# Kernel optimization log

Measured on AMD Instinct MI355X. Metric: run time of the kernel, lower is better.

Reference implementation:

```python
import jax, jax.numpy as jnp
import numpy as np

LMAX = 4
NUM_COEF = (LMAX + 1) ** 2  # 25 spherical-harmonic coefficients
EPS = 1e-5
# degree l of each coefficient index m
DEG = np.repeat(np.arange(LMAX + 1), 2 * np.arange(LMAX + 1) + 1)
# degree-balanced weights for layer_norm_sh (std_balance_degrees=True): 1/((2l+1)*lmax)
_BW = np.zeros(NUM_COEF - 1, dtype=np.float32)
for l in range(1, LMAX + 1):
    _BW[l**2 - 1 : l**2 - 1 + 2 * l + 1] = 1.0 / (2 * l + 1)
_BW /= LMAX


def setup_inputs() -> dict:
    N, C, H, O, S = 20000, 64, 64, 64, 64
    key = jax.random.key(0)
    ks = jax.random.split(key, 9)
    def g(k, shape, scale=0.05):
        return jax.random.normal(k, shape, dtype=jnp.float32) * scale
    return {
        'x': jax.random.normal(ks[0], (N, NUM_COEF, C), dtype=jnp.float32),
        'norm_l0_w': jnp.ones((C,), jnp.float32),
        'norm_l0_b': jnp.zeros((C,), jnp.float32),
        'norm_aff_w': jnp.ones((LMAX, C), jnp.float32),
        'lin1_w': g(ks[1], (LMAX + 1, C, H)),
        'lin1_b': jnp.zeros((H,), jnp.float32),
        'scalar_w': g(ks[2], (C, H)),
        'scalar_b': jnp.zeros((H,), jnp.float32),
        'grid_w1': g(ks[3], (H, 2 * H)),
        'grid_w2': g(ks[4], (2 * H, 2 * H)),
        'grid_w3': g(ks[5], (2 * H, H)),
        'lin2_w': g(ks[6], (LMAX + 1, H, O)),
        'lin2_b': jnp.zeros((O,), jnp.float32),
        'to_grid_mat': g(ks[7], (S, NUM_COEF), scale=0.2),
    }


def reference(x, norm_l0_w, norm_l0_b, norm_aff_w, lin1_w, lin1_b,
              scalar_w, scalar_b, grid_w1, grid_w2, grid_w3,
              lin2_w, lin2_b, to_grid_mat):
    deg = jnp.asarray(DEG)
    bw = jnp.asarray(_BW)
    # --- layer_norm_sh (EquivariantLayerNormArraySphericalHarmonics) ---
    x0 = x[:, :1, :]                                   # [N,1,C] l=0 part
    mu = x0.mean(-1, keepdims=True)
    var = ((x0 - mu) ** 2).mean(-1, keepdims=True)
    x0n = (x0 - mu) * jax.lax.rsqrt(var + EPS) * norm_l0_w + norm_l0_b
    xl = x[:, 1:, :]                                   # [N,24,C] l>=1 part
    fnorm = jnp.einsum('nic,i->nc', xl * xl, bw)[:, None, :]   # degree-balanced RMS
    inv = jax.lax.rsqrt(fnorm.mean(-1, keepdims=True) + EPS)   # [N,1,1]
    xl = xl * inv * norm_aff_w[deg[1:] - 1][None]              # per-degree affine
    xn = jnp.concatenate([x0n, xl], axis=1)            # [N,25,C]
    # --- scalar gating MLP on l=0 (use_grid_mlp + use_sep_s2_act) ---
    gating = jax.nn.silu(jnp.einsum('noc,ch->noh', xn[:, :1, :], scalar_w) + scalar_b)
    # --- SO3_LinearV2 #1: per-degree block-diagonal linear ---
    h = jnp.einsum('nmi,mio->nmo', xn, lin1_w[deg])    # [N,25,H]
    h = h.at[:, 0, :].add(lin1_b)
    # --- grid MLP: to S2 grid, pointwise MLP, back to coefficients ---
    g = jnp.einsum('sm,nmh->nsh', to_grid_mat, h)      # [N,S,H]
    g = jax.nn.silu(g @ grid_w1)
    g = jax.nn.silu(g @ grid_w2)
    g = g @ grid_w3
    h = jnp.einsum('sm,nsh->nmh', to_grid_mat, g)      # from_grid_mat == to_grid_mat
    # --- separable S2 activation: replace l=0 row with gated scalars ---
    h = jnp.concatenate([gating, h[:, 1:, :]], axis=1)
    # --- SO3_LinearV2 #2 ---
    out = jnp.einsum('nmi,mio->nmo', h, lin2_w[deg])   # [N,25,O]
    out = out.at[:, 0, :].add(lin2_b)
    return out
```

## Files before the change

kernel.cpp:

```cpp
#include <hip/hip_runtime.h>
#include <hip/hip_bf16.h>

#define EPSV 1e-5f

typedef __attribute__((ext_vector_type(8))) short short8;
typedef __attribute__((ext_vector_type(4))) float f32x4;

__device__ __forceinline__ int deg_of(int m) {
  return (m == 0) ? 0 : (m < 4 ? 1 : (m < 9 ? 2 : (m < 16 ? 3 : 4)));
}
__device__ __forceinline__ float silu_f(float v) { return v / (1.f + __expf(-v)); }
__device__ __forceinline__ unsigned short f2bf(float v) {
  unsigned int u = __float_as_uint(v);
  return (unsigned short)((u + 0x7FFFu + ((u >> 16) & 1u)) >> 16);
}
__device__ __forceinline__ short bfs(float v) { return (short)f2bf(v); }

#define OFF_L1 0
#define OFF_L2 20480
#define OFF_SC 40960
#define OFF_G1 45056
#define OFF_G2 53248
#define OFF_G3 69632
#define OFF_TG 77824
#define OFF_TGT 79872
#define WS_SHORTS 81920

__global__ __launch_bounds__(256) void prep_weights_kernel(
    const float* __restrict__ l1w, const float* __restrict__ l2w,
    const float* __restrict__ scw, const float* __restrict__ gw1,
    const float* __restrict__ gw2, const float* __restrict__ gw3,
    const float* __restrict__ tgm, short* __restrict__ wsh)
{
  int i = blockIdx.x * 256 + threadIdx.x;
  if (i < 20480) {
    int l = i >> 12, r = i & 4095, h = r >> 6, c = r & 63;
    wsh[i] = bfs(l1w[l * 4096 + c * 64 + h]);
  } else if (i < 40960) {
    int r0 = i - OFF_L2;
    int l = r0 >> 12, r = r0 & 4095, o = r >> 6, h = r & 63;
    wsh[i] = bfs(l2w[l * 4096 + h * 64 + o]);
  } else if (i < 45056) {
    int r = i - OFF_SC, h = r >> 6, c = r & 63;
    wsh[i] = bfs(scw[c * 64 + h]);
  } else if (i < 53248) {
    int r = i - OFF_G1, o = r >> 6, h = r & 63;
    wsh[i] = bfs(gw1[h * 128 + o]);
  } else if (i < 69632) {
    int r = i - OFF_G2, o = r >> 7, h = r & 127;
    wsh[i] = bfs(gw2[h * 128 + o]);
  } else if (i < 77824) {
    int r = i - OFF_G3, o = r >> 7, h = r & 127;
    wsh[i] = bfs(gw3[h * 64 + o]);
  } else if (i < 79872) {
    int r = i - OFF_TG, s = r >> 5, m = r & 31;
    wsh[i] = (m < 25) ? bfs(tgm[s * 25 + m]) : (short)0;
  } else if (i < WS_SHORTS) {
    int r = i - OFF_TGT, m = r >> 6, s = r & 63;
    wsh[i] = (m < 25) ? bfs(tgm[s * 25 + m]) : (short)0;
  }
}


__global__ __launch_bounds__(256, 4) void fused_sample_kernel(
    const float* __restrict__ x,
    const float* __restrict__ nl0w, const float* __restrict__ nl0b,
    const float* __restrict__ affw,
    const float* __restrict__ l1b,
    const float* __restrict__ scb,
    const float* __restrict__ l2b,
    const short* __restrict__ wsh,
    float* __restrict__ out, int nTot)
{
  __shared__ float sm[9856];
  float*          XB  = sm;
  unsigned short* T1u = (unsigned short*)sm;
  unsigned short* G3u = (unsigned short*)sm;
  unsigned short* XBh = (unsigned short*)(sm + 4352);
  unsigned short* H1u = (unsigned short*)(sm + 5504);
  unsigned short* GBu = (unsigned short*)(sm + 6784);
  unsigned short* T2u = (unsigned short*)(sm + 4352);
  float*          RD  = sm + 8704;
  unsigned short* HBh = (unsigned short*)(sm + 8704);

  const int t = threadIdx.x;
  const int n = blockIdx.x;
  if (n >= nTot) return;

  const int W    = t >> 6;
  const int lane = t & 63;
  const int quad = lane >> 4;
  const int l16  = lane & 15;
  const int hcol = W * 16 + l16;

  const float* gx = x + (size_t)n * 1600;
  const short8 z8 = (short8){0,0,0,0,0,0,0,0};

  const short* l1T = wsh + OFF_L1;
  const short* l2T = wsh + OFF_L2;
  const short* scT = wsh + OFF_SC;
  const short* g1T = wsh + OFF_G1;
  const short* g2T = wsh + OFF_G2;
  const short* g3T = wsh + OFF_G3;
  const short* tgP = wsh + OFF_TG;
  const short* tgT = wsh + OFF_TGT;

  for (int f = 4 * t; f < 1600; f += 1024) {
    float4 v = *(const float4*)(gx + f);
    int m = f >> 6, c = f & 63;
    *(float4*)(XB + m * 68 + c) = v;
  }
  for (int i = t; i < 448; i += 256) {
    int r = i / 7, k = 25 + i % 7;
    H1u[r * 40 + k] = 0;
  }
  __syncthreads();

  {
    float part = 0.f;
    for (int f = 64 + t; f < 1600; f += 256) {
      int m = f >> 6, c = f & 63;
      float v = XB[m * 68 + c];
      int l = deg_of(m);
      part += v * v * (1.f / (float)((2 * l + 1) * 4));
    }
    RD[t] = part;
  }
  __syncthreads();
  if (t < 64) {
    float s4 = RD[t] + RD[t + 64] + RD[t + 128] + RD[t + 192];
    #pragma unroll
    for (int o = 32; o >= 1; o >>= 1) s4 += __shfl_xor(s4, o, 64);
    if (t == 0) RD[0] = rsqrtf(s4 * (1.f / 64.f) + EPSV);
  } else if (t < 128) {
    int c = t - 64;
    float v = XB[c];
    float s1 = v, s2 = v * v;
    #pragma unroll
    for (int o = 32; o >= 1; o >>= 1) {
      s1 += __shfl_xor(s1, o, 64);
      s2 += __shfl_xor(s2, o, 64);
    }
    float mu  = s1 * (1.f / 64.f);
    float var = s2 * (1.f / 64.f) - mu * mu;
    XB[c] = (v - mu) * rsqrtf(var + EPSV) * nl0w[c] + nl0b[c];
  }
  __syncthreads();

  short8 B3[12];
  {
    #pragma unroll
    for (int l = 0; l < 5; ++l)
      #pragma unroll
      for (int ks = 0; ks < 2; ++ks)
        B3[l * 2 + ks] = *(const short8*)(l1T + l * 4096 + hcol * 64 + ks * 32 + quad * 8);
    #pragma unroll
    for (int ks = 0; ks < 2; ++ks)
      B3[10 + ks] = *(const short8*)(scT + hcol * 64 + ks * 32 + quad * 8);

    float inv = RD[0];
    for (int f = t; f < 1600; f += 256) {
      int m = f >> 6, c = f & 63;
      float v = XB[m * 68 + c];
      if (m > 0) v *= inv * affw[(deg_of(m) - 1) * 64 + c];
      XBh[m * 72 + c] = f2bf(v);
    }
  }
  __syncthreads();

  float gval;
  short8 tg3b;
  {
    tg3b = *(const short8*)(tgP + (W * 16 + l16) * 32 + quad * 8);

    short8 a0[2], a1[2];
    #pragma unroll
    for (int ks = 0; ks < 2; ++ks) {
      a0[ks] = *(const short8*)(XBh + l16 * 72 + ks * 32 + quad * 8);
      a1[ks] = *(const short8*)(XBh + (16 + l16) * 72 + ks * 32 + quad * 8);
    }
    const int dl = deg_of(l16);
    f32x4 c0 = (f32x4){0,0,0,0}, c1 = (f32x4){0,0,0,0}, cg = (f32x4){0,0,0,0};
    #pragma unroll
    for (int ks = 0; ks < 2; ++ks) {
      #pragma unroll
      for (int l = 0; l < 4; ++l) {
        short8 am = (dl == l) ? a0[ks] : z8;
        c0 = __builtin_amdgcn_mfma_f32_16x16x32_bf16(am, B3[l * 2 + ks], c0, 0, 0, 0);
      }
      c1 = __builtin_amdgcn_mfma_f32_16x16x32_bf16(a1[ks], B3[8 + ks], c1, 0, 0, 0);
      short8 ag = (l16 == 0) ? a0[ks] : z8;
      cg = __builtin_amdgcn_mfma_f32_16x16x32_bf16(ag, B3[10 + ks], cg, 0, 0, 0);
    }
    #pragma unroll
    for (int r = 0; r < 4; ++r) {
      int m = quad * 4 + r;
      float v = c0[r] + ((m == 0) ? l1b[hcol] : 0.f);
      H1u[hcol * 40 + m] = f2bf(v);
    }
    #pragma unroll
    for (int r = 0; r < 4; ++r) {
      int m = 16 + quad * 4 + r;
      if (m < 25) H1u[hcol * 40 + m] = f2bf(c1[r]);
    }
    gval = silu_f(cg[0] + scb[hcol]);
  }
  __syncthreads();

  short8 bf4[4];
  {
    #pragma unroll
    for (int nt2 = 0; nt2 < 2; ++nt2)
      #pragma unroll
      for (int ks = 0; ks < 2; ++ks)
        bf4[nt2 * 2 + ks] = *(const short8*)(g1T + ((2 * W + nt2) * 16 + l16) * 64 + ks * 32 + quad * 8);

    f32x4 cg3[4];
    #pragma unroll
    for (int nt = 0; nt < 4; ++nt) cg3[nt] = (f32x4){0,0,0,0};
    #pragma unroll
    for (int nt = 0; nt < 4; ++nt) {
      short8 b = *(const short8*)(H1u + (nt * 16 + l16) * 40 + quad * 8);
      cg3[nt] = __builtin_amdgcn_mfma_f32_16x16x32_bf16(tg3b, b, cg3[nt], 0, 0, 0);
    }
    #pragma unroll
    for (int nt = 0; nt < 4; ++nt)
      #pragma unroll
      for (int r = 0; r < 4; ++r) {
        int s = W * 16 + quad * 4 + r;
        GBu[s * 72 + nt * 16 + l16] = f2bf(cg3[nt][r]);
      }
  }
  __syncthreads();

  short8 bf5[8];
  {
    #pragma unroll
    for (int nt2 = 0; nt2 < 2; ++nt2)
      #pragma unroll
      for (int ks = 0; ks < 4; ++ks)
        bf5[nt2 * 4 + ks] = *(const short8*)(g2T + ((2 * W + nt2) * 16 + l16) * 128 + ks * 32 + quad * 8);

    f32x4 acc[8];
    #pragma unroll
    for (int i = 0; i < 8; ++i) acc[i] = (f32x4){0,0,0,0};
    #pragma unroll
    for (int mt = 0; mt < 4; ++mt)
      #pragma unroll
      for (int ks = 0; ks < 2; ++ks) {
        short8 a = *(const short8*)(GBu + (mt * 16 + l16) * 72 + ks * 32 + quad * 8);
        acc[mt * 2 + 0] = __builtin_amdgcn_mfma_f32_16x16x32_bf16(a, bf4[ks],     acc[mt * 2 + 0], 0, 0, 0);
        acc[mt * 2 + 1] = __builtin_amdgcn_mfma_f32_16x16x32_bf16(a, bf4[2 + ks], acc[mt * 2 + 1], 0, 0, 0);
      }
    #pragma unroll
    for (int mt = 0; mt < 4; ++mt)
      #pragma unroll
      for (int nt2 = 0; nt2 < 2; ++nt2) {
        int col = (2 * W + nt2) * 16 + l16;
        #pragma unroll
        for (int r = 0; r < 4; ++r) {
          int srow = mt * 16 + quad * 4 + r;
          T1u[srow * 136 + col] = f2bf(silu_f(acc[mt * 2 + nt2][r]));
        }
      }
  }
  __syncthreads();

  short8 bf6[4];
  {
    #pragma unroll
    for (int ks = 0; ks < 4; ++ks)
      bf6[ks] = *(const short8*)(g3T + hcol * 128 + ks * 32 + quad * 8);

    f32x4 acc[8];
    #pragma unroll
    for (int i = 0; i < 8; ++i) acc[i] = (f32x4){0,0,0,0};
    #pragma unroll
    for (int mt = 0; mt < 4; ++mt)
      #pragma unroll
      for (int ks = 0; ks < 4; ++ks) {
        short8 a = *(const short8*)(T1u + (mt * 16 + l16) * 136 + ks * 32 + quad * 8);
        acc[mt * 2 + 0] = __builtin_amdgcn_mfma_f32_16x16x32_bf16(a, bf5[ks],     acc[mt * 2 + 0], 0, 0, 0);
        acc[mt * 2 + 1] = __builtin_amdgcn_mfma_f32_16x16x32_bf16(a, bf5[4 + ks], acc[mt * 2 + 1], 0, 0, 0);
      }
    #pragma unroll
    for (int mt = 0; mt < 4; ++mt)
      #pragma unroll
      for (int nt2 = 0; nt2 < 2; ++nt2) {
        int col = (2 * W + nt2) * 16 + l16;
        #pragma unroll
        for (int r = 0; r < 4; ++r) {
          int srow = mt * 16 + quad * 4 + r;
          T2u[srow * 136 + col] = f2bf(silu_f(acc[mt * 2 + nt2][r]));
        }
      }
  }
  __syncthreads();

  short8 a7[2][2];
  {
    #pragma unroll
    for (int mt = 0; mt < 2; ++mt)
      #pragma unroll
      for (int ks = 0; ks < 2; ++ks)
        a7[mt][ks] = *(const short8*)(tgT + (mt * 16 + l16) * 64 + ks * 32 + quad * 8);

    f32x4 acc[4];
    #pragma unroll
    for (int i = 0; i < 4; ++i) acc[i] = (f32x4){0,0,0,0};
    #pragma unroll
    for (int mt = 0; mt < 4; ++mt)
      #pragma unroll
      for (int ks = 0; ks < 4; ++ks) {
        short8 a = *(const short8*)(T2u + (mt * 16 + l16) * 136 + ks * 32 + quad * 8);
        acc[mt] = __builtin_amdgcn_mfma_f32_16x16x32_bf16(a, bf6[ks], acc[mt], 0, 0, 0);
      }
    #pragma unroll
    for (int mt = 0; mt < 4; ++mt)
      #pragma unroll
      for (int r = 0; r < 4; ++r) {
        int s = mt * 16 + quad * 4 + r;
        G3u[hcol * 72 + s] = f2bf(acc[mt][r]);
      }
  }
  __syncthreads();

  short8 B8[10];
  {
    #pragma unroll
    for (int l = 0; l < 5; ++l)
      #pragma unroll
      for (int ks = 0; ks < 2; ++ks)
        B8[l * 2 + ks] = *(const short8*)(l2T + l * 4096 + hcol * 64 + ks * 32 + quad * 8);

    short8 b7[2];
    #pragma unroll
    for (int ks = 0; ks < 2; ++ks)
      b7[ks] = *(const short8*)(G3u + hcol * 72 + ks * 32 + quad * 8);
    f32x4 c7[2];
    #pragma unroll
    for (int mt = 0; mt < 2; ++mt) c7[mt] = (f32x4){0,0,0,0};
    #pragma unroll
    for (int mt = 0; mt < 2; ++mt)
      #pragma unroll
      for (int ks = 0; ks < 2; ++ks)
        c7[mt] = __builtin_amdgcn_mfma_f32_16x16x32_bf16(a7[mt][ks], b7[ks], c7[mt], 0, 0, 0);
    #pragma unroll
    for (int mt = 0; mt < 2; ++mt)
      #pragma unroll
      for (int r = 0; r < 4; ++r) {
        int m = mt * 16 + quad * 4 + r;
        if (m >= 1 && m < 25) HBh[m * 72 + hcol] = f2bf(c7[mt][r]);
      }
    if (quad == 0) HBh[hcol] = f2bf(gval);
  }
  __syncthreads();

  {
    short8 a0[2], a1[2];
    #pragma unroll
    for (int ks = 0; ks < 2; ++ks) {
      a0[ks] = *(const short8*)(HBh + l16 * 72 + ks * 32 + quad * 8);
      a1[ks] = *(const short8*)(HBh + (16 + l16) * 72 + ks * 32 + quad * 8);
    }
    const int dl = deg_of(l16);
    f32x4 c0 = (f32x4){0,0,0,0}, c1 = (f32x4){0,0,0,0};
    #pragma unroll
    for (int ks = 0; ks < 2; ++ks) {
      #pragma unroll
      for (int l = 0; l < 4; ++l) {
        short8 am = (dl == l) ? a0[ks] : z8;
        c0 = __builtin_amdgcn_mfma_f32_16x16x32_bf16(am, B8[l * 2 + ks], c0, 0, 0, 0);
      }
      c1 = __builtin_amdgcn_mfma_f32_16x16x32_bf16(a1[ks], B8[8 + ks], c1, 0, 0, 0);
    }
    float* go = out + (size_t)n * 1600;
    float bias = l2b[hcol];
    #pragma unroll
    for (int r = 0; r < 4; ++r) {
      int m = quad * 4 + r;
      go[m * 64 + hcol] = c0[r] + ((m == 0) ? bias : 0.f);
    }
    #pragma unroll
    for (int r = 0; r < 4; ++r) {
      int m = 16 + quad * 4 + r;
      if (m < 25) go[m * 64 + hcol] = c1[r];
    }
  }
}

extern "C" void kernel_launch(void* const* d_in, const int* in_sizes, int n_in,
                              void* d_out, int out_size, void* d_ws, size_t ws_size,
                              hipStream_t stream) {
  const float* x    = (const float*)d_in[0];
  const float* nl0w = (const float*)d_in[1];
  const float* nl0b = (const float*)d_in[2];
  const float* affw = (const float*)d_in[3];
  const float* l1w  = (const float*)d_in[4];
  const float* l1b  = (const float*)d_in[5];
  const float* scw  = (const float*)d_in[6];
  const float* scb  = (const float*)d_in[7];
  const float* gw1  = (const float*)d_in[8];
  const float* gw2  = (const float*)d_in[9];
  const float* gw3  = (const float*)d_in[10];
  const float* l2w  = (const float*)d_in[11];
  const float* l2b  = (const float*)d_in[12];
  const float* tgm  = (const float*)d_in[13];

  short* wsh = (short*)d_ws;
  int N = in_sizes[0] / 1600;

  prep_weights_kernel<<<dim3(WS_SHORTS / 256), dim3(256), 0, stream>>>(
      l1w, l2w, scw, gw1, gw2, gw3, tgm, wsh);

  fused_sample_kernel<<<dim3(N), dim3(256), 0, stream>>>(
      x, nl0w, nl0b, affw, l1b, scb, l2b, wsh, (float*)d_out, N);
}
```

Measured before the change: 617.2 us.

## Swap MFMA operand roles so outputs pack into vectorized LDS and global stores

Several MFMA stages swap their A and B operands so each lane's four accumulator values land in consecutive columns. Results can then be packed into paired bf16 words and written with 8-byte LDS stores and 16-byte global stores instead of scalar 2-byte and 4-byte stores. The normalization loops are also vectorized to float4 LDS reads. Padding rows of XBh and HBh are zeroed, because the swapped final stage now reads rows 25 to 31 as B operands. This aims to cut LDS store instruction count and improve global write coalescing, at the cost of more careful padding and indexing.

```diff
diff --git a/kernel.cpp b/kernel.cpp
--- a/kernel.cpp
+++ b/kernel.cpp
@@ -5,6 +5,7 @@
 
 typedef __attribute__((ext_vector_type(8))) short short8;
 typedef __attribute__((ext_vector_type(4))) float f32x4;
+typedef __attribute__((ext_vector_type(2))) unsigned int u32x2;
 
 __device__ __forceinline__ int deg_of(int m) {
   return (m == 0) ? 0 : (m < 4 ? 1 : (m < 9 ? 2 : (m < 16 ? 3 : 4)));
@@ -15,6 +16,9 @@
   return (unsigned short)((u + 0x7FFFu + ((u >> 16) & 1u)) >> 16);
 }
 __device__ __forceinline__ short bfs(float v) { return (short)f2bf(v); }
+__device__ __forceinline__ unsigned int pk2(float a, float b) {
+  return (unsigned int)f2bf(a) | ((unsigned int)f2bf(b) << 16);
+}
 
 #define OFF_L1 0
 #define OFF_L2 20480
@@ -114,15 +118,25 @@
     int r = i / 7, k = 25 + i % 7;
     H1u[r * 40 + k] = 0;
   }
+  for (int i = t; i < 504; i += 256)
+    XBh[25 * 72 + i] = 0;
+  for (int i = t; i < 504; i += 256)
+    HBh[25 * 72 + i] = 0;
   __syncthreads();
 
   {
     float part = 0.f;
-    for (int f = 64 + t; f < 1600; f += 256) {
-      int m = f >> 6, c = f & 63;
-      float v = XB[m * 68 + c];
-      int l = deg_of(m);
-      part += v * v * (1.f / (float)((2 * l + 1) * 4));
+    #pragma unroll
+    for (int it = 0; it < 2; ++it) {
+      int i = t + it * 256;
+      if (i < 384) {
+        int f = 64 + 4 * i;
+        int m = f >> 6, c = f & 63;
+        f32x4 v = *(const f32x4*)(XB + m * 68 + c);
+        int l = deg_of(m);
+        float w = 1.f / (float)((2 * l + 1) * 4);
+        part += (v[0]*v[0] + v[1]*v[1] + v[2]*v[2] + v[3]*v[3]) * w;
+      }
     }
     RD[t] = part;
   }
@@ -159,11 +173,20 @@
       B3[10 + ks] = *(const short8*)(scT + hcol * 64 + ks * 32 + quad * 8);
 
     float inv = RD[0];
-    for (int f = t; f < 1600; f += 256) {
-      int m = f >> 6, c = f & 63;
-      float v = XB[m * 68 + c];
-      if (m > 0) v *= inv * affw[(deg_of(m) - 1) * 64 + c];
-      XBh[m * 72 + c] = f2bf(v);
+    #pragma unroll
+    for (int it = 0; it < 2; ++it) {
+      int i = t + it * 256;
+      if (i < 400) {
+        int m = i >> 4, c = (i & 15) * 4;
+        f32x4 v = *(const f32x4*)(XB + m * 68 + c);
+        if (m > 0) {
+          f32x4 aw = *(const f32x4*)(affw + (deg_of(m) - 1) * 64 + c);
+          v[0] *= inv * aw[0]; v[1] *= inv * aw[1];
+          v[2] *= inv * aw[2]; v[3] *= inv * aw[3];
+        }
+        u32x2 w; w[0] = pk2(v[0], v[1]); w[1] = pk2(v[2], v[3]);
+        *(u32x2*)(XBh + m * 72 + c) = w;
+      }
     }
   }
   __syncthreads();
@@ -192,76 +215,71 @@
       short8 ag = (l16 == 0) ? a0[ks] : z8;
       cg = __builtin_amdgcn_mfma_f32_16x16x32_bf16(ag, B3[10 + ks], cg, 0, 0, 0);
     }
-    #pragma unroll
-    for (int r = 0; r < 4; ++r) {
-      int m = quad * 4 + r;
-      float v = c0[r] + ((m == 0) ? l1b[hcol] : 0.f);
-      H1u[hcol * 40 + m] = f2bf(v);
-    }
-    #pragma unroll
-    for (int r = 0; r < 4; ++r) {
-      int m = 16 + quad * 4 + r;
-      if (m < 25) H1u[hcol * 40 + m] = f2bf(c1[r]);
+    if (quad == 0) c0[0] += l1b[hcol];
+    u32x2 w0; w0[0] = pk2(c0[0], c0[1]); w0[1] = pk2(c0[2], c0[3]);
+    *(u32x2*)(H1u + hcol * 40 + quad * 4) = w0;
+    if (quad < 2) {
+      u32x2 w1; w1[0] = pk2(c1[0], c1[1]); w1[1] = pk2(c1[2], c1[3]);
+      *(u32x2*)(H1u + hcol * 40 + 16 + quad * 4) = w1;
+    } else if (quad == 2) {
+      H1u[hcol * 40 + 24] = f2bf(c1[0]);
     }
     gval = silu_f(cg[0] + scb[hcol]);
   }
   __syncthreads();
 
-  short8 bf4[4];
+  short8 a4w[2][2];
   {
     #pragma unroll
     for (int nt2 = 0; nt2 < 2; ++nt2)
       #pragma unroll
       for (int ks = 0; ks < 2; ++ks)
-        bf4[nt2 * 2 + ks] = *(const short8*)(g1T + ((2 * W + nt2) * 16 + l16) * 64 + ks * 32 + quad * 8);
+        a4w[nt2][ks] = *(const short8*)(g1T + ((2 * W + nt2) * 16 + l16) * 64 + ks * 32 + quad * 8);
 
     f32x4 cg3[4];
     #pragma unroll
     for (int nt = 0; nt < 4; ++nt) cg3[nt] = (f32x4){0,0,0,0};
     #pragma unroll
     for (int nt = 0; nt < 4; ++nt) {
-      short8 b = *(const short8*)(H1u + (nt * 16 + l16) * 40 + quad * 8);
-      cg3[nt] = __builtin_amdgcn_mfma_f32_16x16x32_bf16(tg3b, b, cg3[nt], 0, 0, 0);
-    }
-    #pragma unroll
-    for (int nt = 0; nt < 4; ++nt)
-      #pragma unroll
-      for (int r = 0; r < 4; ++r) {
-        int s = W * 16 + quad * 4 + r;
-        GBu[s * 72 + nt * 16 + l16] = f2bf(cg3[nt][r]);
-      }
-  }
-  __syncthreads();
-
-  short8 bf5[8];
+      short8 ah = *(const short8*)(H1u + (nt * 16 + l16) * 40 + quad * 8);
+      cg3[nt] = __builtin_amdgcn_mfma_f32_16x16x32_bf16(ah, tg3b, cg3[nt], 0, 0, 0);
+    }
+    #pragma unroll
+    for (int nt = 0; nt < 4; ++nt) {
+      u32x2 w; w[0] = pk2(cg3[nt][0], cg3[nt][1]); w[1] = pk2(cg3[nt][2], cg3[nt][3]);
+      *(u32x2*)(GBu + (W * 16 + l16) * 72 + nt * 16 + quad * 4) = w;
+    }
+  }
+  __syncthreads();
+
+  short8 a5w[2][4];
   {
     #pragma unroll
     for (int nt2 = 0; nt2 < 2; ++nt2)
       #pragma unroll
       for (int ks = 0; ks < 4; ++ks)
-        bf5[nt2 * 4 + ks] = *(const short8*)(g2T + ((2 * W + nt2) * 16 + l16) * 128 + ks * 32 + quad * 8);
+        a5w[nt2][ks] = *(const short8*)(g2T + ((2 * W + nt2) * 16 + l16) * 128 + ks * 32 + quad * 8);
 
     f32x4 acc[8];
     #pragma unroll
     for (int i = 0; i < 8; ++i) acc[i] = (f32x4){0,0,0,0};
     #pragma unroll
-    for (int mt = 0; mt < 4; ++mt)
+    for (int st = 0; st < 4; ++st)
       #pragma unroll
       for (int ks = 0; ks < 2; ++ks) {
-        short8 a = *(const short8*)(GBu + (mt * 16 + l16) * 72 + ks * 32 + quad * 8);
-        acc[mt * 2 + 0] = __builtin_amdgcn_mfma_f32_16x16x32_bf16(a, bf4[ks],     acc[mt * 2 + 0], 0, 0, 0);
-        acc[mt * 2 + 1] = __builtin_amdgcn_mfma_f32_16x16x32_bf16(a, bf4[2 + ks], acc[mt * 2 + 1], 0, 0, 0);
-      }
-    #pragma unroll
-    for (int mt = 0; mt < 4; ++mt)
-      #pragma unroll
-      for (int nt2 = 0; nt2 < 2; ++nt2) {
-        int col = (2 * W + nt2) * 16 + l16;
+        short8 b = *(const short8*)(GBu + (st * 16 + l16) * 72 + ks * 32 + quad * 8);
+        acc[0 * 4 + st] = __builtin_amdgcn_mfma_f32_16x16x32_bf16(a4w[0][ks], b, acc[0 * 4 + st], 0, 0, 0);
+        acc[1 * 4 + st] = __builtin_amdgcn_mfma_f32_16x16x32_bf16(a4w[1][ks], b, acc[1 * 4 + st], 0, 0, 0);
+      }
+    #pragma unroll
+    for (int nt2 = 0; nt2 < 2; ++nt2)
+      #pragma unroll
+      for (int st = 0; st < 4; ++st) {
+        f32x4 v = acc[nt2 * 4 + st];
         #pragma unroll
-        for (int r = 0; r < 4; ++r) {
-          int srow = mt * 16 + quad * 4 + r;
-          T1u[srow * 136 + col] = f2bf(silu_f(acc[mt * 2 + nt2][r]));
-        }
+        for (int r = 0; r < 4; ++r) v[r] = silu_f(v[r]);
+        u32x2 w; w[0] = pk2(v[0], v[1]); w[1] = pk2(v[2], v[3]);
+        *(u32x2*)(T1u + (st * 16 + l16) * 136 + (2 * W + nt2) * 16 + quad * 4) = w;
       }
   }
   __syncthreads();
@@ -276,34 +294,33 @@
     #pragma unroll
     for (int i = 0; i < 8; ++i) acc[i] = (f32x4){0,0,0,0};
     #pragma unroll
-    for (int mt = 0; mt < 4; ++mt)
+    for (int st = 0; st < 4; ++st)
       #pragma unroll
       for (int ks = 0; ks < 4; ++ks) {
-        short8 a = *(const short8*)(T1u + (mt * 16 + l16) * 136 + ks * 32 + quad * 8);
-        acc[mt * 2 + 0] = __builtin_amdgcn_mfma_f32_16x16x32_bf16(a, bf5[ks],     acc[mt * 2 + 0], 0, 0, 0);
-        acc[mt * 2 + 1] = __builtin_amdgcn_mfma_f32_16x16x32_bf16(a, bf5[4 + ks], acc[mt * 2 + 1], 0, 0, 0);
-      }
-    #pragma unroll
-    for (int mt = 0; mt < 4; ++mt)
-      #pragma unroll
-      for (int nt2 = 0; nt2 < 2; ++nt2) {
-        int col = (2 * W + nt2) * 16 + l16;
+        short8 b = *(const short8*)(T1u + (st * 16 + l16) * 136 + ks * 32 + quad * 8);
+        acc[0 * 4 + st] = __builtin_amdgcn_mfma_f32_16x16x32_bf16(a5w[0][ks], b, acc[0 * 4 + st], 0, 0, 0);
+        acc[1 * 4 + st] = __builtin_amdgcn_mfma_f32_16x16x32_bf16(a5w[1][ks], b, acc[1 * 4 + st], 0, 0, 0);
+      }
+    #pragma unroll
+    for (int nt2 = 0; nt2 < 2; ++nt2)
+      #pragma unroll
+      for (int st = 0; st < 4; ++st) {
+        f32x4 v = acc[nt2 * 4 + st];
         #pragma unroll
-        for (int r = 0; r < 4; ++r) {
-          int srow = mt * 16 + quad * 4 + r;
-          T2u[srow * 136 + col] = f2bf(silu_f(acc[mt * 2 + nt2][r]));
-        }
-      }
-  }
-  __syncthreads();
-
-  short8 a7[2][2];
+        for (int r = 0; r < 4; ++r) v[r] = silu_f(v[r]);
+        u32x2 w; w[0] = pk2(v[0], v[1]); w[1] = pk2(v[2], v[3]);
+        *(u32x2*)(T2u + (st * 16 + l16) * 136 + (2 * W + nt2) * 16 + quad * 4) = w;
+      }
+  }
+  __syncthreads();
+
+  short8 b7w[2][2];
   {
     #pragma unroll
     for (int mt = 0; mt < 2; ++mt)
       #pragma unroll
       for (int ks = 0; ks < 2; ++ks)
-        a7[mt][ks] = *(const short8*)(tgT + (mt * 16 + l16) * 64 + ks * 32 + quad * 8);
+        b7w[mt][ks] = *(const short8*)(tgT + (mt * 16 + l16) * 64 + ks * 32 + quad * 8);
 
     f32x4 acc[4];
     #pragma unroll
@@ -316,12 +333,10 @@
         acc[mt] = __builtin_amdgcn_mfma_f32_16x16x32_bf16(a, bf6[ks], acc[mt], 0, 0, 0);
       }
     #pragma unroll
-    for (int mt = 0; mt < 4; ++mt)
-      #pragma unroll
-      for (int r = 0; r < 4; ++r) {
-        int s = mt * 16 + quad * 4 + r;
-        G3u[hcol * 72 + s] = f2bf(acc[mt][r]);
-      }
+    for (int mt = 0; mt < 4; ++mt) {
+      u32x2 w; w[0] = pk2(acc[mt][0], acc[mt][1]); w[1] = pk2(acc[mt][2], acc[mt][3]);
+      *(u32x2*)(G3u + hcol * 72 + mt * 16 + quad * 4) = w;
+    }
   }
   __syncthreads();
 
@@ -333,35 +348,32 @@
       for (int ks = 0; ks < 2; ++ks)
         B8[l * 2 + ks] = *(const short8*)(l2T + l * 4096 + hcol * 64 + ks * 32 + quad * 8);
 
-    short8 b7[2];
-    #pragma unroll
-    for (int ks = 0; ks < 2; ++ks)
-      b7[ks] = *(const short8*)(G3u + hcol * 72 + ks * 32 + quad * 8);
     f32x4 c7[2];
-    #pragma unroll
-    for (int mt = 0; mt < 2; ++mt) c7[mt] = (f32x4){0,0,0,0};
-    #pragma unroll
-    for (int mt = 0; mt < 2; ++mt)
-      #pragma unroll
-      for (int ks = 0; ks < 2; ++ks)
-        c7[mt] = __builtin_amdgcn_mfma_f32_16x16x32_bf16(a7[mt][ks], b7[ks], c7[mt], 0, 0, 0);
-    #pragma unroll
-    for (int mt = 0; mt < 2; ++mt)
-      #pragma unroll
-      for (int r = 0; r < 4; ++r) {
-        int m = mt * 16 + quad * 4 + r;
-        if (m >= 1 && m < 25) HBh[m * 72 + hcol] = f2bf(c7[mt][r]);
-      }
+    c7[0] = (f32x4){0,0,0,0}; c7[1] = (f32x4){0,0,0,0};
+    #pragma unroll
+    for (int ks = 0; ks < 2; ++ks) {
+      short8 ag = *(const short8*)(G3u + hcol * 72 + ks * 32 + quad * 8);
+      c7[0] = __builtin_amdgcn_mfma_f32_16x16x32_bf16(ag, b7w[0][ks], c7[0], 0, 0, 0);
+      c7[1] = __builtin_amdgcn_mfma_f32_16x16x32_bf16(ag, b7w[1][ks], c7[1], 0, 0, 0);
+    }
+    if (l16 >= 1) {
+      u32x2 w; w[0] = pk2(c7[0][0], c7[0][1]); w[1] = pk2(c7[0][2], c7[0][3]);
+      *(u32x2*)(HBh + l16 * 72 + W * 16 + quad * 4) = w;
+    }
+    if (l16 < 9) {
+      u32x2 w; w[0] = pk2(c7[1][0], c7[1][1]); w[1] = pk2(c7[1][2], c7[1][3]);
+      *(u32x2*)(HBh + (16 + l16) * 72 + W * 16 + quad * 4) = w;
+    }
     if (quad == 0) HBh[hcol] = f2bf(gval);
   }
   __syncthreads();
 
   {
-    short8 a0[2], a1[2];
+    short8 b0[2], b1[2];
     #pragma unroll
     for (int ks = 0; ks < 2; ++ks) {
-      a0[ks] = *(const short8*)(HBh + l16 * 72 + ks * 32 + quad * 8);
-      a1[ks] = *(const short8*)(HBh + (16 + l16) * 72 + ks * 32 + quad * 8);
+      b0[ks] = *(const short8*)(HBh + l16 * 72 + ks * 32 + quad * 8);
+      b1[ks] = *(const short8*)(HBh + (16 + l16) * 72 + ks * 32 + quad * 8);
     }
     const int dl = deg_of(l16);
     f32x4 c0 = (f32x4){0,0,0,0}, c1 = (f32x4){0,0,0,0};
@@ -369,23 +381,19 @@
     for (int ks = 0; ks < 2; ++ks) {
       #pragma unroll
       for (int l = 0; l < 4; ++l) {
-        short8 am = (dl == l) ? a0[ks] : z8;
-        c0 = __builtin_amdgcn_mfma_f32_16x16x32_bf16(am, B8[l * 2 + ks], c0, 0, 0, 0);
-      }
-      c1 = __builtin_amdgcn_mfma_f32_16x16x32_bf16(a1[ks], B8[8 + ks], c1, 0, 0, 0);
+        short8 bm = (dl == l) ? b0[ks] : z8;
+        c0 = __builtin_amdgcn_mfma_f32_16x16x32_bf16(B8[l * 2 + ks], bm, c0, 0, 0, 0);
+      }
+      c1 = __builtin_amdgcn_mfma_f32_16x16x32_bf16(B8[8 + ks], b1[ks], c1, 0, 0, 0);
     }
     float* go = out + (size_t)n * 1600;
-    float bias = l2b[hcol];
-    #pragma unroll
-    for (int r = 0; r < 4; ++r) {
-      int m = quad * 4 + r;
-      go[m * 64 + hcol] = c0[r] + ((m == 0) ? bias : 0.f);
-    }
-    #pragma unroll
-    for (int r = 0; r < 4; ++r) {
-      int m = 16 + quad * 4 + r;
-      if (m < 25) go[m * 64 + hcol] = c1[r];
-    }
+    if (l16 == 0) {
+      f32x4 l2bv = *(const f32x4*)(l2b + W * 16 + quad * 4);
+      c0[0] += l2bv[0]; c0[1] += l2bv[1]; c0[2] += l2bv[2]; c0[3] += l2bv[3];
+    }
+    *(f32x4*)(go + l16 * 64 + W * 16 + quad * 4) = c0;
+    if (l16 < 9)
+      *(f32x4*)(go + (16 + l16) * 64 + W * 16 + quad * 4) = c1;
   }
 }
 
```

New measurement: 607.3 us. Within noise of the previous version (-1.6%).
